# Performance work log

Hardware: AMD Instinct MI355X
Metric: run time of the kernel (lower is better)

## Reference

```python
import jax, jax.numpy as jnp
import numpy as np

B, N, D, H, C = 32, 128, 32, 64, 10
P = 2 * H + 1  # pair feature dim


def setup_inputs() -> dict:
    key = jax.random.key(0)
    ks = jax.random.split(key, 20)
    f32 = jnp.float32

    def w(k, i, o):
        return (jax.random.normal(k, (i, o), f32) / np.sqrt(i)).astype(f32)

    def bvec(k, o):
        return (jax.random.normal(k, (o,), f32) * 0.02).astype(f32)

    return {
        "x": jax.random.normal(ks[0], (B, N, D), f32),
        "adj": jax.random.uniform(ks[1], (B, N, N), f32),
        # 1-GNN layer 1 (D->H): W1 self, W2 neighbor
        "w11": w(ks[2], D, H), "b11": bvec(ks[3], H),
        "w12": w(ks[4], D, H), "b12": bvec(ks[5], H),
        # 1-GNN layer 2 (H->H)
        "w21": w(ks[6], H, H), "b21": bvec(ks[7], H),
        "w22": w(ks[8], H, H), "b22": bvec(ks[9], H),
        # 2-GNN layer 1 (P->H)
        "p1w1": w(ks[10], P, H), "p1b1": bvec(ks[11], H),
        "p1w2": w(ks[12], P, H), "p1b2": bvec(ks[13], H),
        # 2-GNN layer 2 (H->H)
        "p2w1": w(ks[14], H, H), "p2b1": bvec(ks[15], H),
        "p2w2": w(ks[16], H, H), "p2b2": bvec(ks[17], H),
        # classifier (2H -> C)
        "cw": w(ks[18], 2 * H, C), "cb": bvec(ks[19], C),
    }


def _lin(h, W, b):
    return h @ W + b


def _forward(x, adj, w11, b11, w12, b12, w21, b21, w22, b22,
             p1w1, p1b1, p1w2, p1b2, p2w1, p2b1, p2w2, p2b2, cw, cb):
    n = x.shape[1]
    # ---- dense 1-GNN: h = relu(W1 h + A W2 h) ----
    h = jax.nn.relu(_lin(x, w11, b11) + jnp.einsum('bij,bjd->bid', adj, _lin(x, w12, b12)))
    h = jax.nn.relu(_lin(h, w21, b21) + jnp.einsum('bij,bjd->bid', adj, _lin(h, w22, b22)))
    emb1 = h.sum(axis=1)  # [B,H]

    # ---- dense 2-GNN ----
    eye = jnp.eye(n, dtype=adj.dtype)
    adj_clean = adj * (1.0 - eye)[None]  # zero diagonal
    ii, jj = jnp.meshgrid(jnp.arange(n), jnp.arange(n), indexing='ij')
    imin = jnp.minimum(ii, jj)  # canonical min-index node of pair
    imax = jnp.maximum(ii, jj)
    first = h[:, imin, :]   # [B,N,N,H] = h at min(i,j)
    second = h[:, imax, :]  # [B,N,N,H] = h at max(i,j)
    pair = jnp.concatenate([first, second, adj_clean[..., None]], axis=-1)  # [B,N,N,P]

    for (W1, b1, W2, b2) in ((p1w1, p1b1, p1w2, p1b2), (p2w1, p2b1, p2w2, p2b2)):
        g = _lin(pair, W2, b2)          # [B,N,N,H]
        self_part = _lin(pair, W1, b1)  # [B,N,N,H]
        agg1 = jnp.einsum('biw,bjwd->bijd', adj_clean, g)
        agg2 = jnp.einsum('bjw,biwd->bijd', adj_clean, g)
        pair = jax.nn.relu(self_part + agg1 + agg2)

    upper = jnp.triu(jnp.ones((n, n), dtype=pair.dtype), k=1)
    emb2 = (pair * upper[None, :, :, None]).sum(axis=(1, 2))  # [B,H]

    return jnp.concatenate([emb1, emb2], axis=1) @ cw + cb  # [B,C]


def reference(x, adj, w11, b11, w12, b12, w21, b21, w22, b22,
              p1w1, p1b1, p1w2, p1b2, p2w1, p2b1, p2w2, p2b2, cw, cb):
    return _forward(x, adj, w11, b11, w12, b12, w21, b21, w22, b22,
                    p1w1, p1b1, p1w2, p1b2, p2w1, p2b1, p2w2, p2b2, cw, cb)
```

## Files before the change

kernel.cpp:

```cpp
#include <hip/hip_runtime.h>

#define B 32
#define N 128
#define DD 32
#define H 64
#define C 10

typedef unsigned short bfu;
typedef __attribute__((ext_vector_type(8))) short bf16x8;
typedef __attribute__((ext_vector_type(4))) float f32x4;

#define MFMA16 __builtin_amdgcn_mfma_f32_16x16x32_bf16

__device__ __forceinline__ float b2f(bfu v) {
    union { unsigned u; float f; } x; x.u = ((unsigned)v) << 16; return x.f;
}
__device__ __forceinline__ bfu f2b(float f) {
    union { __bf16 b; bfu u; } c; c.b = (__bf16)f; return c.u;
}
__device__ __forceinline__ float lo2f(unsigned u) {
    union { unsigned x; float f; } c; c.x = u << 16; return c.f;
}
__device__ __forceinline__ float hi2f(unsigned u) {
    union { unsigned x; float f; } c; c.x = u & 0xffff0000u; return c.f;
}
__device__ __forceinline__ void up8(uint4 u, float* f) {
    f[0] = lo2f(u.x); f[1] = hi2f(u.x); f[2] = lo2f(u.y); f[3] = hi2f(u.y);
    f[4] = lo2f(u.z); f[5] = hi2f(u.z); f[6] = lo2f(u.w); f[7] = hi2f(u.w);
}
__device__ __forceinline__ unsigned pk2(float a, float b) {
    return (unsigned)f2b(a) | ((unsigned)f2b(b) << 16);
}

struct WT { const float* src[10]; bfu* dst[10]; int K[10]; };
__global__ __launch_bounds__(256) void prep_all(const float* __restrict__ adj,
                                                bfu* __restrict__ acb,
                                                bfu* __restrict__ adjf, WT p) {
    int blk = blockIdx.x;
    if (blk < 512) {
        int idx = blk * 256 + threadIdx.x;
        float4 v = ((const float4*)adj)[idx];
        int e0 = idx * 4;
        int w = e0 & 127;
        int i = (e0 >> 7) & 127;
        ushort4 o;
        o.x = f2b((i == w    ) ? 0.f : v.x);
        o.y = f2b((i == w + 1) ? 0.f : v.y);
        o.z = f2b((i == w + 2) ? 0.f : v.z);
        o.w = f2b((i == w + 3) ? 0.f : v.w);
        ((ushort4*)acb)[idx] = o;
        ushort4 oF;
        oF.x = f2b(v.x); oF.y = f2b(v.y); oF.z = f2b(v.z); oF.w = f2b(v.w);
        ((ushort4*)adjf)[idx] = oF;
    } else {
        int m = blk - 512;
        const float* S = p.src[m];
        bfu* D = p.dst[m];
        int K = p.K[m];
        int t = threadIdx.x; int d = t & 63;
        for (int k = t >> 6; k < K; k += 4)
            D[d * K + k] = f2b(S[k * 64 + d]);
    }
}

__global__ __launch_bounds__(256) void gnn_front(const float* __restrict__ x,
                                                 const bfu* __restrict__ adjf,
                                                 const bfu* __restrict__ w11t,
                                                 const float* __restrict__ b11,
                                                 const bfu* __restrict__ w12t,
                                                 const float* __restrict__ b12,
                                                 const bfu* __restrict__ w21t,
                                                 const float* __restrict__ b21,
                                                 const bfu* __restrict__ w22t,
                                                 const float* __restrict__ b22,
                                                 const bfu* __restrict__ u1t,
                                                 const bfu* __restrict__ v1t,
                                                 const bfu* __restrict__ u2t,
                                                 const bfu* __restrict__ v2t,
                                                 bfu* __restrict__ U1,
                                                 bfu* __restrict__ V1,
                                                 bfu* __restrict__ U2,
                                                 bfu* __restrict__ V2,
                                                 float* __restrict__ emb1) {
    int b = blockIdx.x;
    int t = threadIdx.x, lane = t & 63, wid = t >> 6;
    int l16 = lane & 15, g4 = lane >> 4;
    __shared__ bfu Af[128 * 136];
    __shared__ bfu Yt[64 * 136];
    __shared__ bfu Hs[128 * 72];
    __shared__ bfu Xs[128 * 40];
    __shared__ float red[16][64];
    {
        int i = t >> 1, half = t & 1;
        const uint4* src = (const uint4*)(adjf + ((size_t)b * N + i) * N + half * 64);
        uint4* dst = (uint4*)&Af[i * 136 + half * 64];
#pragma unroll
        for (int q = 0; q < 8; ++q) dst[q] = src[q];
        const float4* sx = (const float4*)(x + ((size_t)b * N + i) * DD + half * 16);
        float xv[16];
        *(float4*)&xv[0]  = sx[0]; *(float4*)&xv[4]  = sx[1];
        *(float4*)&xv[8]  = sx[2]; *(float4*)&xv[12] = sx[3];
        unsigned q[8];
#pragma unroll
        for (int e = 0; e < 8; ++e) q[e] = pk2(xv[2 * e], xv[2 * e + 1]);
        uint4* dx = (uint4*)&Xs[i * 40 + half * 16];
        dx[0] = make_uint4(q[0], q[1], q[2], q[3]);
        dx[1] = make_uint4(q[4], q[5], q[6], q[7]);
    }
    __syncthreads();
    f32x4 a1[2][4], a2[2][4];
#define ZERO(A) _Pragma("unroll") for (int m = 0; m < 2; ++m) _Pragma("unroll") for (int n = 0; n < 4; ++n) A[m][n] = (f32x4){0.f,0.f,0.f,0.f};
    ZERO(a1); ZERO(a2);
    {
        int k0 = g4 * 8;
        bf16x8 bw1[4], bw2[4];
#pragma unroll
        for (int n = 0; n < 4; ++n) {
            bw1[n] = *(const bf16x8*)&w11t[(l16 + 16 * n) * 32 + k0];
            bw2[n] = *(const bf16x8*)&w12t[(l16 + 16 * n) * 32 + k0];
        }
#pragma unroll
        for (int m = 0; m < 2; ++m) {
            bf16x8 afr = *(const bf16x8*)&Xs[(wid * 32 + m * 16 + l16) * 40 + k0];
#pragma unroll
            for (int n = 0; n < 4; ++n) {
                a1[m][n] = MFMA16(afr, bw1[n], a1[m][n], 0, 0, 0);
                a2[m][n] = MFMA16(afr, bw2[n], a2[m][n], 0, 0, 0);
            }
        }
    }
    {
        float bb[4];
#pragma unroll
        for (int n = 0; n < 4; ++n) bb[n] = b12[l16 + 16 * n];
#pragma unroll
        for (int m = 0; m < 2; ++m)
#pragma unroll
            for (int n = 0; n < 4; ++n) {
                uint2 q;
                q.x = pk2(a2[m][n][0] + bb[n], a2[m][n][1] + bb[n]);
                q.y = pk2(a2[m][n][2] + bb[n], a2[m][n][3] + bb[n]);
                *(uint2*)&Yt[(l16 + 16 * n) * 136 + wid * 32 + m * 16 + g4 * 4] = q;
            }
    }
    __syncthreads();
    ZERO(a2);
#pragma unroll
    for (int ks = 0; ks < 4; ++ks) {
        int k0 = ks * 32 + g4 * 8;
        bf16x8 bfr[4];
#pragma unroll
        for (int n = 0; n < 4; ++n) bfr[n] = *(const bf16x8*)&Yt[(l16 + 16 * n) * 136 + k0];
#pragma unroll
        for (int m = 0; m < 2; ++m) {
            bf16x8 afr = *(const bf16x8*)&Af[(wid * 32 + m * 16 + l16) * 136 + k0];
#pragma unroll
            for (int n = 0; n < 4; ++n) a2[m][n] = MFMA16(afr, bfr[n], a2[m][n], 0, 0, 0);
        }
    }
    {
        float bb[4];
#pragma unroll
        for (int n = 0; n < 4; ++n) bb[n] = b11[l16 + 16 * n];
#pragma unroll
        for (int m = 0; m < 2; ++m)
#pragma unroll
            for (int n = 0; n < 4; ++n)
#pragma unroll
                for (int r = 0; r < 4; ++r)
                    Hs[(wid * 32 + m * 16 + g4 * 4 + r) * 72 + l16 + 16 * n] =
                        f2b(fmaxf(a1[m][n][r] + bb[n] + a2[m][n][r], 0.f));
    }
    __syncthreads();
    ZERO(a1); ZERO(a2);
#pragma unroll
    for (int ks = 0; ks < 2; ++ks) {
        int k0 = ks * 32 + g4 * 8;
        bf16x8 bw1[4], bw2[4];
#pragma unroll
        for (int n = 0; n < 4; ++n) {
            bw1[n] = *(const bf16x8*)&w21t[(l16 + 16 * n) * 64 + k0];
            bw2[n] = *(const bf16x8*)&w22t[(l16 + 16 * n) * 64 + k0];
        }
#pragma unroll
        for (int m = 0; m < 2; ++m) {
            bf16x8 afr = *(const bf16x8*)&Hs[(wid * 32 + m * 16 + l16) * 72 + k0];
#pragma unroll
            for (int n = 0; n < 4; ++n) {
                a1[m][n] = MFMA16(afr, bw1[n], a1[m][n], 0, 0, 0);
                a2[m][n] = MFMA16(afr, bw2[n], a2[m][n], 0, 0, 0);
            }
        }
    }
    {
        float bb[4];
#pragma unroll
        for (int n = 0; n < 4; ++n) bb[n] = b22[l16 + 16 * n];
#pragma unroll
        for (int m = 0; m < 2; ++m)
#pragma unroll
            for (int n = 0; n < 4; ++n) {
                uint2 q;
                q.x = pk2(a2[m][n][0] + bb[n], a2[m][n][1] + bb[n]);
                q.y = pk2(a2[m][n][2] + bb[n], a2[m][n][3] + bb[n]);
                *(uint2*)&Yt[(l16 + 16 * n) * 136 + wid * 32 + m * 16 + g4 * 4] = q;
            }
    }
    __syncthreads();
    ZERO(a2);
#pragma unroll
    for (int ks = 0; ks < 4; ++ks) {
        int k0 = ks * 32 + g4 * 8;
        bf16x8 bfr[4];
#pragma unroll
        for (int n = 0; n < 4; ++n) bfr[n] = *(const bf16x8*)&Yt[(l16 + 16 * n) * 136 + k0];
#pragma unroll
        for (int m = 0; m < 2; ++m) {
            bf16x8 afr = *(const bf16x8*)&Af[(wid * 32 + m * 16 + l16) * 136 + k0];
#pragma unroll
            for (int n = 0; n < 4; ++n) a2[m][n] = MFMA16(afr, bfr[n], a2[m][n], 0, 0, 0);
        }
    }
    {
        float bb[4], s[4] = {0.f, 0.f, 0.f, 0.f};
#pragma unroll
        for (int n = 0; n < 4; ++n) bb[n] = b21[l16 + 16 * n];
#pragma unroll
        for (int m = 0; m < 2; ++m)
#pragma unroll
            for (int n = 0; n < 4; ++n)
#pragma unroll
                for (int r = 0; r < 4; ++r) {
                    float v = fmaxf(a1[m][n][r] + bb[n] + a2[m][n][r], 0.f);
                    Hs[(wid * 32 + m * 16 + g4 * 4 + r) * 72 + l16 + 16 * n] = f2b(v);
                    s[n] += v;
                }
#pragma unroll
        for (int n = 0; n < 4; ++n) red[wid * 4 + g4][l16 + 16 * n] = s[n];
    }
    __syncthreads();
    if (t < 64) {
        float e = 0.f;
#pragma unroll
        for (int q = 0; q < 16; ++q) e += red[q][t];
        emb1[b * 64 + t] = e;
    }
    const bfu* wts[4] = {u1t, v1t, u2t, v2t};
    bfu* outs[4] = {U1, V1, U2, V2};
#pragma unroll
    for (int o = 0; o < 4; ++o) {
        ZERO(a1);
#pragma unroll
        for (int ks = 0; ks < 2; ++ks) {
            int k0 = ks * 32 + g4 * 8;
            bf16x8 bw[4];
#pragma unroll
            for (int n = 0; n < 4; ++n)
                bw[n] = *(const bf16x8*)&wts[o][(l16 + 16 * n) * 64 + k0];
#pragma unroll
            for (int m = 0; m < 2; ++m) {
                bf16x8 afr = *(const bf16x8*)&Hs[(wid * 32 + m * 16 + l16) * 72 + k0];
#pragma unroll
                for (int n = 0; n < 4; ++n) a1[m][n] = MFMA16(afr, bw[n], a1[m][n], 0, 0, 0);
            }
        }
#pragma unroll
        for (int m = 0; m < 2; ++m)
#pragma unroll
            for (int n = 0; n < 4; ++n)
#pragma unroll
                for (int r = 0; r < 4; ++r)
                    Af[(wid * 32 + m * 16 + g4 * 4 + r) * 72 + l16 + 16 * n] = f2b(a1[m][n][r]);
        __syncthreads();
        {
            int i = t >> 1, half = t & 1;
            const uint4* src = (const uint4*)&Af[i * 72 + half * 32];
            uint4* dst = (uint4*)(outs[o] + ((size_t)b * N + i) * H + half * 32);
            dst[0] = src[0]; dst[1] = src[1]; dst[2] = src[2]; dst[3] = src[3];
        }
        __syncthreads();
    }
#undef ZERO
}

__device__ __forceinline__ int xcd_swz(int wg, int nwg) {
    return (wg & 7) * (nwg >> 3) + (wg >> 3);
}

__global__ __launch_bounds__(256) void t1_mfma(const bfu* __restrict__ U2,
                                               const bfu* __restrict__ V2,
                                               const bfu* __restrict__ acb,
                                               const float* __restrict__ wl,
                                               const float* __restrict__ bv,
                                               bfu* __restrict__ T, int b0) {
    int wid2 = xcd_swz(blockIdx.x, gridDim.x);
    int bl = wid2 >> 7, j = wid2 & 127;
    int b = b0 + bl;
    int t = threadIdx.x, lane = t & 63, wid = t >> 6;
    int l16 = lane & 15, g4 = lane >> 4;
    __shared__ bfu lds[128 * 72];
    __shared__ float arl[N];
    const bfu* arow = acb + ((size_t)b * N + j) * N;
    if (t < N) arl[t] = b2f(arow[t]);
    __syncthreads();
    {
        int d = lane;
        const bfu* U2b = U2 + (size_t)b * N * H;
        const bfu* V2b = V2 + (size_t)b * N * H;
        float wld = wl[d], bvd = bv[d];
        float UjB = b2f(U2b[j * H + d]) + bvd, VjB = b2f(V2b[j * H + d]) + bvd;
#pragma unroll
        for (int p = 0; p < 4; ++p) {
            int w0 = p * 32 + wid * 8;
            unsigned q[4];
#pragma unroll
            for (int rr = 0; rr < 4; ++rr) {
                float g01[2];
#pragma unroll
                for (int hh = 0; hh < 2; ++hh) {
                    int w = w0 + rr * 2 + hh;
                    float a = arl[w];
                    float rvar = (w < j) ? b2f(U2b[w * H + d]) : b2f(V2b[w * H + d]);
                    float base = (w < j) ? VjB : UjB;
                    g01[hh] = rvar + base + a * wld;
                }
                q[rr] = pk2(g01[0], g01[1]);
            }
            *(uint4*)&lds[d * 136 + w0] = make_uint4(q[0], q[1], q[2], q[3]);
        }
    }
    __syncthreads();
    f32x4 acc[2][4];
#pragma unroll
    for (int m = 0; m < 2; ++m)
#pragma unroll
        for (int n = 0; n < 4; ++n) acc[m][n] = (f32x4){0.f, 0.f, 0.f, 0.f};
    const bfu* Ab = acb + (size_t)b * N * N;
#pragma unroll
    for (int ks = 0; ks < 4; ++ks) {
        int k0 = ks * 32 + g4 * 8;
        bf16x8 bfr[4];
#pragma unroll
        for (int n = 0; n < 4; ++n)
            bfr[n] = *(const bf16x8*)&lds[(l16 + 16 * n) * 136 + k0];
#pragma unroll
        for (int m = 0; m < 2; ++m) {
            int i = wid * 32 + m * 16 + l16;
            bf16x8 afr = *(const bf16x8*)&Ab[(size_t)i * N + k0];
#pragma unroll
            for (int n = 0; n < 4; ++n)
                acc[m][n] = MFMA16(afr, bfr[n], acc[m][n], 0, 0, 0);
        }
    }
    __syncthreads();
#pragma unroll
    for (int m = 0; m < 2; ++m)
#pragma unroll
        for (int n = 0; n < 4; ++n)
#pragma unroll
            for (int r = 0; r < 4; ++r)
                lds[(wid * 32 + m * 16 + g4 * 4 + r) * 72 + l16 + 16 * n] = f2b(acc[m][n][r]);
    __syncthreads();
    {
        int i = t >> 1, half = t & 1;
        const uint4* src = (const uint4*)&lds[i * 72 + half * 32];
        uint4* dst = (uint4*)(T + (((size_t)bl * N + j) * N + i) * H + half * 32);
        dst[0] = src[0]; dst[1] = src[1]; dst[2] = src[2]; dst[3] = src[3];
    }
}

__device__ __forceinline__ void build_P2(bfu* Pl, const bfu* U1b,
                                         const bfu* V1b, const bfu* arow,
                                         const bfu* Trow, const bfu* Tcol,
                                         const float* wl1, const float* bv1,
                                         int c, int t) {
    int wq = t >> 3, d0 = (t & 7) * 8;
    float wv[8], bvv[8], UcB[8], VcB[8];
    *(float4*)&wv[0]  = *(const float4*)(wl1 + d0);
    *(float4*)&wv[4]  = *(const float4*)(wl1 + d0 + 4);
    *(float4*)&bvv[0] = *(const float4*)(bv1 + d0);
    *(float4*)&bvv[4] = *(const float4*)(bv1 + d0 + 4);
    up8(*(const uint4*)&U1b[c * H + d0], UcB);
    up8(*(const uint4*)&V1b[c * H + d0], VcB);
#pragma unroll
    for (int e = 0; e < 8; ++e) { UcB[e] += bvv[e]; VcB[e] += bvv[e]; }
#pragma unroll
    for (int p = 0; p < 4; ++p) {
        int w = p * 32 + wq;
        float a = b2f(arow[w]);
        const bfu* rs = (w < c) ? U1b : V1b;
        float rv[8], tc[8], tw[8];
        up8(*(const uint4*)&rs[w * H + d0], rv);
        up8(*(const uint4*)&Trow[(size_t)w * H + d0], tc);
        up8(*(const uint4*)&Tcol[(size_t)w * N * H + d0], tw);
        unsigned q[4];
#pragma unroll
        for (int e = 0; e < 4; ++e) {
            float b0 = (w < c) ? VcB[2 * e] : UcB[2 * e];
            float b1 = (w < c) ? VcB[2 * e + 1] : UcB[2 * e + 1];
            float p0 = fmaxf(rv[2 * e]     + b0 + a * wv[2 * e]     + tc[2 * e]     + tw[2 * e],     0.f);
            float p1 = fmaxf(rv[2 * e + 1] + b1 + a * wv[2 * e + 1] + tc[2 * e + 1] + tw[2 * e + 1], 0.f);
            q[e] = pk2(p0, p1);
        }
        *(uint4*)&Pl[w * 72 + d0] = make_uint4(q[0], q[1], q[2], q[3]);
    }
}

__global__ __launch_bounds__(256) void t2_fused(const bfu* __restrict__ U1,
                                                const bfu* __restrict__ V1,
                                                const bfu* __restrict__ acb,
                                                const float* __restrict__ wl1,
                                                const float* __restrict__ bv1,
                                                const bfu* __restrict__ T1,
                                                const bfu* __restrict__ W2t,
                                                const float* __restrict__ bv2,
                                                bfu* __restrict__ T2, int b0) {
    int wid2 = xcd_swz(blockIdx.x, gridDim.x);
    int bl = wid2 >> 7, j = wid2 & 127;
    int b = b0 + bl;
    int t = threadIdx.x, lane = t & 63, wid = t >> 6;
    int l16 = lane & 15, g4 = lane >> 4;
    __shared__ bfu P[128 * 72];
    __shared__ bfu Gt[64 * 136];
    const bfu* T1b = T1 + (size_t)bl * N * N * H;
    build_P2(P, U1 + (size_t)b * N * H, V1 + (size_t)b * N * H,
             acb + ((size_t)b * N + j) * N,
             T1b + (size_t)j * N * H, T1b + (size_t)j * H,
             wl1, bv1, j, t);
    __syncthreads();
    f32x4 acc[2][4];
#pragma unroll
    for (int m = 0; m < 2; ++m)
#pragma unroll
        for (int n = 0; n < 4; ++n) acc[m][n] = (f32x4){0.f, 0.f, 0.f, 0.f};
#pragma unroll
    for (int ks = 0; ks < 2; ++ks) {
        int k0 = ks * 32 + g4 * 8;
        bf16x8 bw[4];
#pragma unroll
        for (int n = 0; n < 4; ++n)
            bw[n] = *(const bf16x8*)&W2t[(l16 + 16 * n) * 64 + k0];
#pragma unroll
        for (int m = 0; m < 2; ++m) {
            bf16x8 afr = *(const bf16x8*)&P[(wid * 32 + m * 16 + l16) * 72 + k0];
#pragma unroll
            for (int n = 0; n < 4; ++n)
                acc[m][n] = MFMA16(afr, bw[n], acc[m][n], 0, 0, 0);
        }
    }
    {
        float bb[4];
#pragma unroll
        for (int n = 0; n < 4; ++n) bb[n] = bv2[l16 + 16 * n];
#pragma unroll
        for (int m = 0; m < 2; ++m)
#pragma unroll
            for (int n = 0; n < 4; ++n) {
                uint2 q;
                q.x = pk2(acc[m][n][0] + bb[n], acc[m][n][1] + bb[n]);
                q.y = pk2(acc[m][n][2] + bb[n], acc[m][n][3] + bb[n]);
                *(uint2*)&Gt[(l16 + 16 * n) * 136 + wid * 32 + m * 16 + g4 * 4] = q;
            }
    }
    __syncthreads();
#pragma unroll
    for (int m = 0; m < 2; ++m)
#pragma unroll
        for (int n = 0; n < 4; ++n) acc[m][n] = (f32x4){0.f, 0.f, 0.f, 0.f};
    const bfu* Ab = acb + (size_t)b * N * N;
#pragma unroll
    for (int ks = 0; ks < 4; ++ks) {
        int k0 = ks * 32 + g4 * 8;
        bf16x8 bfr[4];
#pragma unroll
        for (int n = 0; n < 4; ++n)
            bfr[n] = *(const bf16x8*)&Gt[(l16 + 16 * n) * 136 + k0];
#pragma unroll
        for (int m = 0; m < 2; ++m) {
            int i = wid * 32 + m * 16 + l16;
            bf16x8 afr = *(const bf16x8*)&Ab[(size_t)i * N + k0];
#pragma unroll
            for (int n = 0; n < 4; ++n)
                acc[m][n] = MFMA16(afr, bfr[n], acc[m][n], 0, 0, 0);
        }
    }
#pragma unroll
    for (int m = 0; m < 2; ++m)
#pragma unroll
        for (int n = 0; n < 4; ++n)
#pragma unroll
            for (int r = 0; r < 4; ++r)
                P[(wid * 32 + m * 16 + g4 * 4 + r) * 72 + l16 + 16 * n] = f2b(acc[m][n][r]);
    __syncthreads();
    {
        int i = t >> 1, half = t & 1;
        const uint4* src = (const uint4*)&P[i * 72 + half * 32];
        uint4* dst = (uint4*)(T2 + (((size_t)bl * N + j) * N + i) * H + half * 32);
        dst[0] = src[0]; dst[1] = src[1]; dst[2] = src[2]; dst[3] = src[3];
    }
}

__global__ __launch_bounds__(256) void combine2_fused(const bfu* __restrict__ U1,
                                                      const bfu* __restrict__ V1,
                                                      const bfu* __restrict__ acb,
                                                      const float* __restrict__ wl1,
                                                      const float* __restrict__ bv1,
                                                      const bfu* __restrict__ T1,
                                                      const bfu* __restrict__ W1t,
                                                      const float* __restrict__ bv2,
                                                      const bfu* __restrict__ T2,
                                                      float* __restrict__ part2, int b0) {
    int wid2 = xcd_swz(blockIdx.x, gridDim.x);
    int bl = wid2 >> 7, i = wid2 & 127;
    int b = b0 + bl;
    int t = threadIdx.x, lane = t & 63, wid = t >> 6;
    int l16 = lane & 15, g4 = lane >> 4;
    __shared__ bfu P[128 * 72];
    __shared__ float red[32][64];
    const bfu* T1b = T1 + (size_t)bl * N * N * H;
    build_P2(P, U1 + (size_t)b * N * H, V1 + (size_t)b * N * H,
             acb + ((size_t)b * N + i) * N,
             T1b + (size_t)i * N * H, T1b + (size_t)i * H,
             wl1, bv1, i, t);
    __syncthreads();
    f32x4 acc[2][4];
#pragma unroll
    for (int m = 0; m < 2; ++m)
#pragma unroll
        for (int n = 0; n < 4; ++n) acc[m][n] = (f32x4){0.f, 0.f, 0.f, 0.f};
#pragma unroll
    for (int ks = 0; ks < 2; ++ks) {
        int k0 = ks * 32 + g4 * 8;
        bf16x8 bw[4];
#pragma unroll
        for (int n = 0; n < 4; ++n)
            bw[n] = *(const bf16x8*)&W1t[(l16 + 16 * n) * 64 + k0];
#pragma unroll
        for (int m = 0; m < 2; ++m) {
            bf16x8 afr = *(const bf16x8*)&P[(wid * 32 + m * 16 + l16) * 72 + k0];
#pragma unroll
            for (int n = 0; n < 4; ++n)
                acc[m][n] = MFMA16(afr, bw[n], acc[m][n], 0, 0, 0);
        }
    }
    {
        float bb[4];
#pragma unroll
        for (int n = 0; n < 4; ++n) bb[n] = bv2[l16 + 16 * n];
#pragma unroll
        for (int m = 0; m < 2; ++m)
#pragma unroll
            for (int n = 0; n < 4; ++n)
#pragma unroll
                for (int r = 0; r < 4; ++r)
                    P[(wid * 32 + m * 16 + g4 * 4 + r) * 72 + l16 + 16 * n] =
                        f2b(acc[m][n][r] + bb[n]);
    }
    __syncthreads();
    int dc = t & 7, jg = t >> 3, d0 = dc * 8;
    float ps[8];
#pragma unroll
    for (int e = 0; e < 8; ++e) ps[e] = 0.f;
    const bfu* T2b = T2 + (size_t)bl * N * N * H;
#pragma unroll
    for (int r = 0; r < 4; ++r) {
        int j = jg + r * 32;
        if (j > i) {
            float ti[8], tj[8], sv[8];
            up8(*(const uint4*)&T2b[((size_t)i * N + j) * H + d0], ti);
            up8(*(const uint4*)&T2b[((size_t)j * N + i) * H + d0], tj);
            up8(*(const uint4*)&P[j * 72 + d0], sv);
#pragma unroll
            for (int e = 0; e < 8; ++e)
                ps[e] += fmaxf(sv[e] + ti[e] + tj[e], 0.f);
        }
    }
#pragma unroll
    for (int e = 0; e < 8; ++e) red[jg][d0 + e] = ps[e];
    __syncthreads();
    if (t < 64) {
        float s = 0.f;
#pragma unroll 8
        for (int g = 0; g < 32; ++g) s += red[g][t];
        part2[((size_t)b * N + i) * H + t] = s;
    }
}

__global__ __launch_bounds__(64) void tail_kernel(const float* __restrict__ part2,
                                                  const float* __restrict__ emb1,
                                                  const float* __restrict__ cw,
                                                  const float* __restrict__ cb,
                                                  float* __restrict__ out) {
    int b = blockIdx.x;
    int d = threadIdx.x;
    __shared__ float e2[64];
    float acc = 0.f;
#pragma unroll 8
    for (int n = 0; n < N; ++n) acc += part2[((size_t)b * N + n) * H + d];
    e2[d] = acc;
    __syncthreads();
    if (d < C) {
        float o = cb[d];
#pragma unroll 8
        for (int k = 0; k < H; ++k) {
            o += emb1[(size_t)b * H + k] * cw[(size_t)k * C + d];
            o += e2[k] * cw[(size_t)(H + k) * C + d];
        }
        out[(size_t)b * C + d] = o;
    }
}

extern "C" void kernel_launch(void* const* d_in, const int* in_sizes, int n_in,
                              void* d_out, int out_size, void* d_ws, size_t ws_size,
                              hipStream_t stream) {
    const float* x    = (const float*)d_in[0];
    const float* adj  = (const float*)d_in[1];
    const float* w11  = (const float*)d_in[2];
    const float* b11  = (const float*)d_in[3];
    const float* w12  = (const float*)d_in[4];
    const float* b12  = (const float*)d_in[5];
    const float* w21  = (const float*)d_in[6];
    const float* b21  = (const float*)d_in[7];
    const float* w22  = (const float*)d_in[8];
    const float* b22  = (const float*)d_in[9];
    const float* p1w1 = (const float*)d_in[10];
    const float* p1b1 = (const float*)d_in[11];
    const float* p1w2 = (const float*)d_in[12];
    const float* p1b2 = (const float*)d_in[13];
    const float* p2w1 = (const float*)d_in[14];
    const float* p2b1 = (const float*)d_in[15];
    const float* p2w2 = (const float*)d_in[16];
    const float* p2b2 = (const float*)d_in[17];
    const float* cw   = (const float*)d_in[18];
    const float* cb   = (const float*)d_in[19];
    float* out = (float*)d_out;

    const size_t NBH = (size_t)B * N * H;
    const size_t BIG = (size_t)N * N * H;

    float* part2 = (float*)d_ws;
    float* emb1  = part2 + NBH;
    float* emb2  = emb1 + (size_t)B * H;
    bfu* U1   = (bfu*)(emb2 + (size_t)B * H);
    bfu* V1   = U1 + NBH;
    bfu* U2   = V1 + NBH;
    bfu* V2   = U2 + NBH;
    bfu* acb  = V2 + NBH;
    bfu* adjf = acb + (size_t)B * N * N;
    bfu* w11t = adjf + (size_t)B * N * N;
    bfu* w12t = w11t + 32 * 64;
    bfu* w21t = w12t + 32 * 64;
    bfu* w22t = w21t + 64 * 64;
    bfu* u1t  = w22t + 64 * 64;
    bfu* v1t  = u1t + 64 * 64;
    bfu* u2t  = v1t + 64 * 64;
    bfu* v2t  = u2t + 64 * 64;
    bfu* W1t  = v2t + 64 * 64;
    bfu* W2t  = W1t + 64 * 64;
    bfu* bigBase = W2t + 64 * 64;
    size_t smallBytes = (char*)bigBase - (char*)d_ws;

    int CB = B;
    while (CB > 1 && smallBytes + 2ull * CB * BIG * sizeof(bfu) > ws_size) CB >>= 1;
    bfu* T1 = bigBase;
    bfu* T2 = T1 + (size_t)CB * BIG;

    {
        WT p;
        const float* srcs[10] = {w11, w12, w21, w22,
                                 p1w1, p1w1 + 64 * H, p1w2, p1w2 + 64 * H,
                                 p2w1, p2w2};
        bfu* dsts[10] = {w11t, w12t, w21t, w22t, u1t, v1t, u2t, v2t, W1t, W2t};
        int Ks[10] = {32, 32, 64, 64, 64, 64, 64, 64, 64, 64};
        for (int q = 0; q < 10; ++q) { p.src[q] = srcs[q]; p.dst[q] = dsts[q]; p.K[q] = Ks[q]; }
        prep_all<<<dim3(512 + 10), 256, 0, stream>>>(adj, acb, adjf, p);
    }
    gnn_front<<<dim3(B), 256, 0, stream>>>(x, adjf, w11t, b11, w12t, b12,
                                           w21t, b21, w22t, b22,
                                           u1t, v1t, u2t, v2t,
                                           U1, V1, U2, V2, emb1);
    for (int b0 = 0; b0 < B; b0 += CB) {
        dim3 cg(CB * N);
        t1_mfma<<<cg, 256, 0, stream>>>(U2, V2, acb, p1w2 + 128 * H, p1b2, T1, b0);
        t2_fused<<<cg, 256, 0, stream>>>(U1, V1, acb, p1w1 + 128 * H, p1b1,
                                         T1, W2t, p2b2, T2, b0);
        combine2_fused<<<cg, 256, 0, stream>>>(U1, V1, acb, p1w1 + 128 * H, p1b1,
                                               T1, W1t, p2b1, T2, part2, b0);
    }
    tail_kernel<<<dim3(B), 64, 0, stream>>>(part2, emb1, cw, cb, out);
}
```

Measured before the change: 165.7 us.

## Compute pair self-part in t2 kernel and slim down the combine kernel

Result: slower. 184.1 us (+11.1%).

```diff
diff --git a/kernel.cpp b/kernel.cpp
--- a/kernel.cpp
+++ b/kernel.cpp
@@ -414,6 +414,9 @@
                                                 const bfu* __restrict__ T1,
                                                 const bfu* __restrict__ W2t,
                                                 const float* __restrict__ bv2,
+                                                const bfu* __restrict__ W1t,
+                                                const float* __restrict__ bvS,
+                                                bfu* __restrict__ Sout,
                                                 bfu* __restrict__ T2, int b0) {
     int wid2 = xcd_swz(blockIdx.x, gridDim.x);
     int bl = wid2 >> 7, j = wid2 & 127;
@@ -428,41 +431,58 @@
              T1b + (size_t)j * N * H, T1b + (size_t)j * H,
              wl1, bv1, j, t);
     __syncthreads();
-    f32x4 acc[2][4];
+    f32x4 acc[2][4], sac[2][4];
 #pragma unroll
     for (int m = 0; m < 2; ++m)
 #pragma unroll
-        for (int n = 0; n < 4; ++n) acc[m][n] = (f32x4){0.f, 0.f, 0.f, 0.f};
+        for (int n = 0; n < 4; ++n) {
+            acc[m][n] = (f32x4){0.f, 0.f, 0.f, 0.f};
+            sac[m][n] = (f32x4){0.f, 0.f, 0.f, 0.f};
+        }
 #pragma unroll
     for (int ks = 0; ks < 2; ++ks) {
         int k0 = ks * 32 + g4 * 8;
-        bf16x8 bw[4];
-#pragma unroll
-        for (int n = 0; n < 4; ++n)
-            bw[n] = *(const bf16x8*)&W2t[(l16 + 16 * n) * 64 + k0];
+        bf16x8 bw2[4], bw1[4];
+#pragma unroll
+        for (int n = 0; n < 4; ++n) {
+            bw2[n] = *(const bf16x8*)&W2t[(l16 + 16 * n) * 64 + k0];
+            bw1[n] = *(const bf16x8*)&W1t[(l16 + 16 * n) * 64 + k0];
+        }
 #pragma unroll
         for (int m = 0; m < 2; ++m) {
             bf16x8 afr = *(const bf16x8*)&P[(wid * 32 + m * 16 + l16) * 72 + k0];
 #pragma unroll
-            for (int n = 0; n < 4; ++n)
-                acc[m][n] = MFMA16(afr, bw[n], acc[m][n], 0, 0, 0);
-        }
-    }
-    {
-        float bb[4];
-#pragma unroll
-        for (int n = 0; n < 4; ++n) bb[n] = bv2[l16 + 16 * n];
+            for (int n = 0; n < 4; ++n) {
+                acc[m][n] = MFMA16(afr, bw2[n], acc[m][n], 0, 0, 0);
+                sac[m][n] = MFMA16(afr, bw1[n], sac[m][n], 0, 0, 0);
+            }
+        }
+    }
+    {
+        float bb2[4], bb1[4];
+#pragma unroll
+        for (int n = 0; n < 4; ++n) { bb2[n] = bv2[l16 + 16 * n]; bb1[n] = bvS[l16 + 16 * n]; }
 #pragma unroll
         for (int m = 0; m < 2; ++m)
 #pragma unroll
             for (int n = 0; n < 4; ++n) {
                 uint2 q;
-                q.x = pk2(acc[m][n][0] + bb[n], acc[m][n][1] + bb[n]);
-                q.y = pk2(acc[m][n][2] + bb[n], acc[m][n][3] + bb[n]);
+                q.x = pk2(acc[m][n][0] + bb2[n], acc[m][n][1] + bb2[n]);
+                q.y = pk2(acc[m][n][2] + bb2[n], acc[m][n][3] + bb2[n]);
                 *(uint2*)&Gt[(l16 + 16 * n) * 136 + wid * 32 + m * 16 + g4 * 4] = q;
-            }
-    }
-    __syncthreads();
+#pragma unroll
+                for (int r = 0; r < 4; ++r)
+                    P[(wid * 32 + m * 16 + g4 * 4 + r) * 72 + l16 + 16 * n] =
+                        f2b(sac[m][n][r] + bb1[n]);
+            }
+    }
+    __syncthreads();
+    {
+        int i = t >> 1, half = t & 1;
+        const uint4* src = (const uint4*)&P[i * 72 + half * 32];
+        uint4* dst = (uint4*)(Sout + (((size_t)bl * N + j) * N + i) * H + half * 32);
+        dst[0] = src[0]; dst[1] = src[1]; dst[2] = src[2]; dst[3] = src[3];
+    }
 #pragma unroll
     for (int m = 0; m < 2; ++m)
 #pragma unroll
@@ -484,6 +504,7 @@
                 acc[m][n] = MFMA16(afr, bfr[n], acc[m][n], 0, 0, 0);
         }
     }
+    __syncthreads();
 #pragma unroll
     for (int m = 0; m < 2; ++m)
 #pragma unroll
@@ -500,76 +521,29 @@
     }
 }
 
-__global__ __launch_bounds__(256) void combine2_fused(const bfu* __restrict__ U1,
-                                                      const bfu* __restrict__ V1,
-                                                      const bfu* __restrict__ acb,
-                                                      const float* __restrict__ wl1,
-                                                      const float* __restrict__ bv1,
-                                                      const bfu* __restrict__ T1,
-                                                      const bfu* __restrict__ W1t,
-                                                      const float* __restrict__ bv2,
-                                                      const bfu* __restrict__ T2,
-                                                      float* __restrict__ part2, int b0) {
+__global__ __launch_bounds__(256) void combine2_lite(const bfu* __restrict__ S,
+                                                     const bfu* __restrict__ T2,
+                                                     float* __restrict__ part2, int b0) {
     int wid2 = xcd_swz(blockIdx.x, gridDim.x);
     int bl = wid2 >> 7, i = wid2 & 127;
     int b = b0 + bl;
-    int t = threadIdx.x, lane = t & 63, wid = t >> 6;
-    int l16 = lane & 15, g4 = lane >> 4;
-    __shared__ bfu P[128 * 72];
+    int t = threadIdx.x;
     __shared__ float red[32][64];
-    const bfu* T1b = T1 + (size_t)bl * N * N * H;
-    build_P2(P, U1 + (size_t)b * N * H, V1 + (size_t)b * N * H,
-             acb + ((size_t)b * N + i) * N,
-             T1b + (size_t)i * N * H, T1b + (size_t)i * H,
-             wl1, bv1, i, t);
-    __syncthreads();
-    f32x4 acc[2][4];
-#pragma unroll
-    for (int m = 0; m < 2; ++m)
-#pragma unroll
-        for (int n = 0; n < 4; ++n) acc[m][n] = (f32x4){0.f, 0.f, 0.f, 0.f};
-#pragma unroll
-    for (int ks = 0; ks < 2; ++ks) {
-        int k0 = ks * 32 + g4 * 8;
-        bf16x8 bw[4];
-#pragma unroll
-        for (int n = 0; n < 4; ++n)
-            bw[n] = *(const bf16x8*)&W1t[(l16 + 16 * n) * 64 + k0];
-#pragma unroll
-        for (int m = 0; m < 2; ++m) {
-            bf16x8 afr = *(const bf16x8*)&P[(wid * 32 + m * 16 + l16) * 72 + k0];
-#pragma unroll
-            for (int n = 0; n < 4; ++n)
-                acc[m][n] = MFMA16(afr, bw[n], acc[m][n], 0, 0, 0);
-        }
-    }
-    {
-        float bb[4];
-#pragma unroll
-        for (int n = 0; n < 4; ++n) bb[n] = bv2[l16 + 16 * n];
-#pragma unroll
-        for (int m = 0; m < 2; ++m)
-#pragma unroll
-            for (int n = 0; n < 4; ++n)
-#pragma unroll
-                for (int r = 0; r < 4; ++r)
-                    P[(wid * 32 + m * 16 + g4 * 4 + r) * 72 + l16 + 16 * n] =
-                        f2b(acc[m][n][r] + bb[n]);
-    }
-    __syncthreads();
     int dc = t & 7, jg = t >> 3, d0 = dc * 8;
+    const bfu* Srow  = S  + ((size_t)bl * N + i) * (size_t)(N * H);
+    const bfu* T2row = T2 + ((size_t)bl * N + i) * (size_t)(N * H);
+    const bfu* T2col = T2 + (size_t)bl * N * N * H + (size_t)i * H;
     float ps[8];
 #pragma unroll
     for (int e = 0; e < 8; ++e) ps[e] = 0.f;
-    const bfu* T2b = T2 + (size_t)bl * N * N * H;
 #pragma unroll
     for (int r = 0; r < 4; ++r) {
         int j = jg + r * 32;
         if (j > i) {
-            float ti[8], tj[8], sv[8];
-            up8(*(const uint4*)&T2b[((size_t)i * N + j) * H + d0], ti);
-            up8(*(const uint4*)&T2b[((size_t)j * N + i) * H + d0], tj);
-            up8(*(const uint4*)&P[j * 72 + d0], sv);
+            float sv[8], ti[8], tj[8];
+            up8(*(const uint4*)&Srow[(size_t)j * H + d0], sv);
+            up8(*(const uint4*)&T2row[(size_t)j * H + d0], ti);
+            up8(*(const uint4*)&T2col[(size_t)j * N * H + d0], tj);
 #pragma unroll
             for (int e = 0; e < 8; ++e)
                 ps[e] += fmaxf(sv[e] + ti[e] + tj[e], 0.f);
@@ -661,9 +635,10 @@
     size_t smallBytes = (char*)bigBase - (char*)d_ws;
 
     int CB = B;
-    while (CB > 1 && smallBytes + 2ull * CB * BIG * sizeof(bfu) > ws_size) CB >>= 1;
+    while (CB > 1 && smallBytes + 3ull * CB * BIG * sizeof(bfu) > ws_size) CB >>= 1;
     bfu* T1 = bigBase;
     bfu* T2 = T1 + (size_t)CB * BIG;
+    bfu* Sb = T2 + (size_t)CB * BIG;
 
     {
         WT p;
@@ -683,9 +658,8 @@
         dim3 cg(CB * N);
         t1_mfma<<<cg, 256, 0, stream>>>(U2, V2, acb, p1w2 + 128 * H, p1b2, T1, b0);
         t2_fused<<<cg, 256, 0, stream>>>(U1, V1, acb, p1w1 + 128 * H, p1b1,
-                                         T1, W2t, p2b2, T2, b0);
-        combine2_fused<<<cg, 256, 0, stream>>>(U1, V1, acb, p1w1 + 128 * H, p1b1,
-                                               T1, W1t, p2b1, T2, part2, b0);
+                                         T1, W2t, p2b2, W1t, p2b1, Sb, T2, b0);
+        combine2_lite<<<cg, 256, 0, stream>>>(Sb, T2, part2, b0);
     }
     tail_kernel<<<dim3(B), 64, 0, stream>>>(part2, emb1, cw, cb, out);
 }
```
